# Optimization experiments

Measured on AMD Instinct MI355X. Metric: run time of the kernel, lower is better.

The kernel has to match this reference:

```python
import jax, jax.numpy as jnp
from jax import lax
import numpy as np

DN = ('NCHW', 'OIHW', 'NCHW')

def _conv(x, w, b, s):
    # torch Conv2d(kernel=3, padding=1, stride=s)
    y = lax.conv_general_dilated(x, w, (s, s), ((1, 1), (1, 1)), dimension_numbers=DN)
    return y + b[None, :, None, None]

def _convT(x, w, b, s):
    # torch ConvTranspose2d weight layout [in, out, kh, kw]; kernel=3, padding=1, output_padding=s-1
    wk = jnp.flip(w, (2, 3)).transpose(1, 0, 2, 3)  # -> OIHW
    y = lax.conv_general_dilated(x, wk, (1, 1), ((1, s), (1, s)), lhs_dilation=(s, s), dimension_numbers=DN)
    return y + b[None, :, None, None]

def _inorm(x, eps=1e-5):
    # torch InstanceNorm2d (affine=False)
    m = jnp.mean(x, (2, 3), keepdims=True)
    v = jnp.var(x, (2, 3), keepdims=True)
    return (x - m) * lax.rsqrt(v + eps)

def _prelu(x, a):
    return jnp.where(x >= 0, x, a * x)

def _block(x, w, b, a, s):
    return _prelu(_inorm(_conv(x, w, b, s)), a)

def _sage(x, src, tgt, wl, bl, wr, n):
    # PyG SAGEConv, mean aggregation: lin_l(scatter_mean(x[src] -> tgt)) + lin_r(x)
    deg = jnp.zeros((n,), x.dtype).at[tgt].add(1.0)
    agg = jnp.zeros((x.shape[0], n, x.shape[2]), x.dtype).at[:, tgt].add(x[:, src])
    agg = agg / jnp.maximum(deg, 1.0)[None, :, None]
    return jnp.einsum('bnc,oc->bno', agg, wl) + bl + jnp.einsum('bnc,oc->bno', x, wr)

def setup_inputs() -> dict:
    keys = iter(jax.random.split(jax.random.key(0), 64))
    def rn(shape, s=0.05):
        return jax.random.normal(next(keys), shape, jnp.float32) * s
    inp = {}
    inp['x'] = jax.random.normal(next(keys), (16, 1, 400, 400), jnp.float32)
    inp['edges'] = jax.random.randint(next(keys), (2, 5000), 0, 625, jnp.int32)
    for name, (ci, co) in zip(['d4', 'd3', 'd2', 'd1'], [(1, 32), (32, 64), (64, 128), (128, 256)]):
        inp['w_' + name] = rn((co, ci, 3, 3)); inp['b_' + name] = rn((co,))
        inp['a_' + name] = jnp.full((1,), 0.25, jnp.float32)
    inp['w_bot'] = rn((256, 256, 3, 3)); inp['b_bot'] = rn((256,))
    inp['a_bot'] = jnp.full((1,), 0.25, jnp.float32)
    for i in ['1', '2']:
        inp['wl' + i] = rn((256, 256)); inp['bl' + i] = rn((256,)); inp['wr' + i] = rn((256, 256))
    for name, (ci, co) in zip(['u1', 'u2', 'u3'], [(512, 128), (256, 64), (128, 32)]):
        inp['w_' + name] = rn((ci, co, 3, 3)); inp['b_' + name] = rn((co,))
        inp['a_' + name] = jnp.full((1,), 0.25, jnp.float32)
    inp['w_u4'] = rn((64, 2, 3, 3)); inp['b_u4'] = rn((2,))
    return inp

def reference(x, edges, w_d4, b_d4, a_d4, w_d3, b_d3, a_d3, w_d2, b_d2, a_d2, w_d1, b_d1, a_d1, w_bot, b_bot, a_bot, wl1, bl1, wr1, wl2, bl2, wr2, w_u1, b_u1, a_u1, w_u2, b_u2, a_u2, w_u3, b_u3, a_u3, w_u4, b_u4):
    xs = []
    x = _block(x, w_d4, b_d4, a_d4, 2); xs.append(x)   # [B,32,200,200]
    x = _block(x, w_d3, b_d3, a_d3, 2); xs.append(x)   # [B,64,100,100]
    x = _block(x, w_d2, b_d2, a_d2, 2); xs.append(x)   # [B,128,50,50]
    x = _block(x, w_d1, b_d1, a_d1, 2); xs.append(x)   # [B,256,25,25]
    x = _block(x, w_bot, b_bot, a_bot, 1)              # [B,256,25,25]
    B = x.shape[0]
    x = x.reshape(B, 256, -1).transpose(0, 2, 1)       # [B,625,256]
    src, tgt = edges[0], edges[1]
    x = jax.nn.relu(_sage(x, src, tgt, wl1, bl1, wr1, 625))
    x = jax.nn.relu(_sage(x, src, tgt, wl2, bl2, wr2, 625))
    x = x.transpose(0, 2, 1).reshape(B, 256, 25, 25)
    x = jnp.concatenate([xs[3], x], 1)                 # 512 ch
    x = _prelu(_inorm(_convT(x, w_u1, b_u1, 2)), a_u1) # [B,128,50,50]
    x = jnp.concatenate([xs[2], x], 1)
    x = _prelu(_inorm(_convT(x, w_u2, b_u2, 2)), a_u2) # [B,64,100,100]
    x = jnp.concatenate([xs[1], x], 1)
    x = _prelu(_inorm(_convT(x, w_u3, b_u3, 2)), a_u3) # [B,32,200,200]
    x = jnp.concatenate([xs[0], x], 1)
    return _convT(x, w_u4, b_u4, 2)                    # [B,2,400,400], conv_only top
```

## Files before the change

### kernel.cpp

```cpp
#include <hip/hip_runtime.h>
#include <hip/hip_bf16.h>

typedef __hip_bfloat16 bf16;

typedef __bf16 bf16x8 __attribute__((ext_vector_type(8)));
typedef float  f32x16 __attribute__((ext_vector_type(16)));

static __device__ __forceinline__ float bf(const bf16 v){ return __bfloat162float(v); }
static __device__ __forceinline__ float bfu(unsigned short u){
  unsigned fw = ((unsigned)u) << 16; float v; __builtin_memcpy(&v, &fw, 4); return v;
}

static __device__ __forceinline__ float ldm(const void* p, long i, int f){
  return f ? ((const float*)p)[i] : __bfloat162float(((const bf16*)p)[i]);
}
static __device__ __forceinline__ void stm(void* p, long i, int f, float v){
  if(f) ((float*)p)[i] = v; else ((bf16*)p)[i] = __float2bfloat16(v);
}
static __device__ __forceinline__ unsigned short bfbits(float v){
  __hip_bfloat16 h = __float2bfloat16(v);
  return *(unsigned short*)&h;
}

__global__ void k_detect(const void* __restrict__ w, int* __restrict__ mode){
  if(blockIdx.x == 0 && threadIdx.x == 0){
    const unsigned int* u = (const unsigned int*)w;
    int saneLo = 0;
    for(int i = 0; i < 64; i++){
      unsigned short lo = (unsigned short)(u[i] & 0xFFFFu);
      unsigned int fw = ((unsigned int)lo) << 16;
      float v; __builtin_memcpy(&v, &fw, 4);
      float a = fabsf(v);
      if(a > 1e-7f && a < 100.f) saneLo++;
    }
    *mode = (saneLo >= 48) ? 0 : 1;
  }
}

__global__ void k_wtrans6(const void* __restrict__ w, bf16* __restrict__ wF,
                          const int* __restrict__ dmode){
  int idx = blockIdx.x * 256 + threadIdx.x;
  if(idx >= 65536) return;
  int dm = *dmode;
  int e = idx & 7;
  int L = (idx >> 3) & 63;
  int r = idx >> 9;
  int nc = r & 7;
  int kc = r >> 3;
  int o = nc*32 + (L & 31);
  int c = kc*16 + (L >> 5)*8 + e;
  wF[idx] = __float2bfloat16(ldm(w, (long)o*256 + c, dm));
}

__global__ void k_wtrans4(const void* __restrict__ w, bf16* __restrict__ wF,
                          const int* __restrict__ dmode, int Cin, int Cout){
  int idx = blockIdx.x * 256 + threadIdx.x;
  if(idx >= Cin * Cout * 9) return;
  int dm = *dmode;
  int e = idx & 7;
  int L = (idx >> 3) & 63;
  int r = idx >> 9;
  int NC = Cout >> 5;
  int nc = r % NC; r /= NC;
  int t  = r % 9;
  int kc = r / 9;
  int ci = kc*16 + (L>>5)*8 + e;
  int co = nc*32 + (L&31);
  wF[idx] = __float2bfloat16(ldm(w, ((long)ci*Cout + co)*9 + t, dm));
}

__global__ void k_wtrans5(const void* __restrict__ w, bf16* __restrict__ wF,
                          const int* __restrict__ dmode, int Cin, int Cout){
  int idx = blockIdx.x * 256 + threadIdx.x;
  if(idx >= Cin * Cout * 9) return;
  int dm = *dmode;
  int e = idx & 7;
  int L = (idx >> 3) & 63;
  int r = idx >> 9;
  int NC = Cout >> 5;
  int nc = r % NC; r /= NC;
  int t  = r % 9;
  int kc = r / 9;
  int ci = kc*16 + (L>>5)*8 + e;
  int co = nc*32 + (L&31);
  wF[idx] = __float2bfloat16(ldm(w, ((long)co*Cin + ci)*9 + t, dm));
}

__global__ __launch_bounds__(256, 4)
void k_conv_d4(const void* __restrict__ in, long in_off,
               const void* __restrict__ w, const void* __restrict__ bias,
               bf16* __restrict__ out, const int* __restrict__ dmode)
{
  __shared__ float sW[288];
  __shared__ float sB[32];
  int tid = threadIdx.x;
  int dm = *dmode;
  for(int e = tid; e < 288; e += 256) sW[e] = ldm(w, e, dm);
  if(tid < 32)  sB[tid] = ldm(bias, tid, dm);
  __syncthreads();
  int r = tid / 50, jt = tid % 50;
  if(r >= 5) return;
  int ho = blockIdx.x * 5 + r;
  int b  = blockIdx.z;
  int j0 = jt * 4;

  float x[3][9];
  long ibase = in_off + (long)b * 160000;
  #pragma unroll
  for(int rr = 0; rr < 3; rr++){
    int ir = 2*ho - 1 + rr;
    if(ir < 0 || ir >= 400){
      #pragma unroll
      for(int c = 0; c < 9; c++) x[rr][c] = 0.f;
      continue;
    }
    long rb = ibase + (long)ir * 400;
    int c0 = 2*j0 - 1;
    #pragma unroll
    for(int c = 0; c < 9; c++){
      int ic = c0 + c;
      x[rr][c] = (ic >= 0 && ic < 400) ? ldm(in, rb + ic, dm) : 0.f;
    }
  }

  long obase = ((long)b * 32) * 40000 + (long)ho * 200 + j0;
  for(int co = 0; co < 32; co++){
    const float* wv = &sW[co*9];
    float bv = sB[co];
    float a[4];
    #pragma unroll
    for(int p = 0; p < 4; p++){
      float s = bv;
      #pragma unroll
      for(int kh = 0; kh < 3; kh++)
        #pragma unroll
        for(int kw = 0; kw < 3; kw++)
          s += x[kh][2*p + kw] * wv[kh*3 + kw];
      a[p] = s;
    }
    ushort4 pk;
    pk.x = bfbits(a[0]); pk.y = bfbits(a[1]); pk.z = bfbits(a[2]); pk.w = bfbits(a[3]);
    *(ushort4*)&out[obase + (long)co * 40000] = pk;
  }
}

template<int CW, int NWC, int NWM, int S, int OCC, int VECW>
__global__ __launch_bounds__(256, OCC)
void k_convSM(const void* __restrict__ in, long in_off, int fin_sel,
              const bf16* __restrict__ wF, const void* __restrict__ bias,
              void* __restrict__ out, int fout,
              const int* __restrict__ dmode,
              int Cin, int Hin, int Win, int Cout, int Hout, int Wout, int nym)
{
  constexpr int CP = 40;
  constexpr int HALF = CW/2;
  __shared__ unsigned short sX[3*CW*CP];
  int tid  = threadIdx.x;
  int lane = tid & 63;
  int wv   = tid >> 6;
  int nc   = wv % NWC;
  int mt   = wv / NWC;
  int ho   = blockIdx.x;
  int colg = blockIdx.y % nym;
  int cog  = blockIdx.y / nym;
  int b    = blockIdx.z;
  int dm   = *dmode;
  int fin  = (fin_sel == 2) ? dm : fin_sel;
  int NCtot = Cout >> 5;
  int chunk = cog*NWC + nc;
  int jl   = mt*32 + (lane & 31);
  int hi   = lane >> 5;
  int C0   = S*(colg*NWM*32);
  int ir0  = S*ho - 1;

  f32x16 acc;
  #pragma unroll
  for(int q = 0; q < 16; q++) acc[q] = 0.f;

  int p0, p1, p2;
  if(S == 2){ p0 = jl; p1 = HALF + jl; p2 = jl + 1; }
  else      { p0 = jl; p1 = jl + 1;    p2 = jl + 2; }

  for(int ci0 = 0; ci0 < Cin; ci0 += 32){
    if(VECW == 1){
      for(int e = tid; e < 12*CW; e += 256){
        int c  = e % CW;
        int s  = e / CW;
        int kg = s & 3, r = s >> 2;
        int ir = ir0 + r;
        int ic = C0 - 1 + c;
        unsigned pk0, pk1, pk2, pk3;
        if(ir >= 0 && ir < Hin && ic >= 0 && ic < Win){
          long step = (long)Hin*Win;
          long base = in_off + ((long)b*Cin + ci0 + kg*8)*step + (long)ir*Win + ic;
          unsigned short t8[8];
          #pragma unroll
          for(int u = 0; u < 8; u++) t8[u] = bfbits(ldm(in, base + u*step, fin));
          pk0 = t8[0] | ((unsigned)t8[1]<<16);
          pk1 = t8[2] | ((unsigned)t8[3]<<16);
          pk2 = t8[4] | ((unsigned)t8[5]<<16);
          pk3 = t8[6] | ((unsigned)t8[7]<<16);
        } else { pk0=0; pk1=0; pk2=0; pk3=0; }
        int pos = (S == 2) ? ((c&1) ? HALF + (c>>1) : (c>>1)) : c;
        uint4 q; q.x=pk0; q.y=pk1; q.z=pk2; q.w=pk3;
        *(uint4*)&sX[(r*CW + pos)*CP + kg*8] = q;
      }
    } else {
      const unsigned short* bp = (const unsigned short*)in;
      long step = (long)Hin*Win;
      int L0 = (C0 >= 1) ? ((C0-1) & ~(VECW-1)) : -VECW;
      int ng = (C0 + CW - 2 - L0)/VECW + 1;
      int total = 3 * 8 * ng;
      for(int e = tid; e < total; e += 256){
        int c4 = e & 7;
        int s  = e >> 3;
        int g  = s % ng;
        int r  = s / ng;
        int ir = ir0 + r;
        int L  = L0 + g*VECW;
        int cib = ci0 + c4*4;
        unsigned short t[4][VECW];
        if(ir >= 0 && ir < Hin && L >= 0 && L + VECW <= Win){
          const unsigned short* rp = bp + in_off + ((long)b*Cin + cib)*step + (long)ir*Win + L;
          #pragma unroll
          for(int u = 0; u < 4; u++){
            if(VECW == 4){
              ushort4 v = *(const ushort4*)(rp + u*step);
              t[u][0]=v.x; t[u][1]=v.y; t[u][2]=v.z; t[u][3]=v.w;
            } else {
              ushort2 v = *(const ushort2*)(rp + u*step);
              t[u][0]=v.x; t[u][1]=v.y;
            }
          }
        } else {
          #pragma unroll
          for(int j = 0; j < VECW; j++){
            int ic = L + j;
            bool ok = (ir >= 0 && ir < Hin && ic >= 0 && ic < Win);
            #pragma unroll
            for(int u = 0; u < 4; u++)
              t[u][j] = ok ? bp[in_off + ((long)b*Cin + cib+u)*step + (long)ir*Win + ic]
                           : (unsigned short)0;
          }
        }
        #pragma unroll
        for(int j = 0; j < VECW; j++){
          int c = L - C0 + 1 + j;
          if(c < 0 || c >= CW) continue;
          int pos = (S == 2) ? ((c&1) ? HALF + (c>>1) : (c>>1)) : c;
          uint2 q;
          q.x = t[0][j] | ((unsigned)t[1][j]<<16);
          q.y = t[2][j] | ((unsigned)t[3][j]<<16);
          *(uint2*)&sX[(r*CW + pos)*CP + c4*4] = q;
        }
      }
    }
    __syncthreads();

    #pragma unroll
    for(int kg2 = 0; kg2 < 2; kg2++){
      int kbase = 8*hi + kg2*16;
      bf16x8 x[9];
      #pragma unroll
      for(int r = 0; r < 3; r++){
        x[r*3+0] = *(const bf16x8*)&sX[(r*CW + p0)*CP + kbase];
        x[r*3+1] = *(const bf16x8*)&sX[(r*CW + p1)*CP + kbase];
        x[r*3+2] = *(const bf16x8*)&sX[(r*CW + p2)*CP + kbase];
      }
      int kc = (ci0 >> 4) + kg2;
      const bf16x8* wb = ((const bf16x8*)wF) + ((long)(kc*9)*NCtot + chunk)*64 + lane;
      const long ws = (long)NCtot*64;
      #pragma unroll
      for(int t = 0; t < 9; t++){
        bf16x8 w = wb[(long)t*ws];
        acc = __builtin_amdgcn_mfma_f32_32x32x16_bf16(w, x[t], acc, 0,0,0);
      }
    }
    __syncthreads();
  }

  int j = colg*NWM*32 + jl;
  if(j < Wout){
    #pragma unroll
    for(int r16 = 0; r16 < 16; r16++){
      int co = chunk*32 + (r16&3) + 8*(r16>>2) + 4*hi;
      float bv = ldm(bias, co, dm);
      stm(out, ((long)b*Cout + co)*Hout*Wout + (long)ho*Wout + j, fout, acc[r16] + bv);
    }
  }
}

__global__ void k_inorm_prelu(void* __restrict__ x, int f, int HW,
                              const void* __restrict__ a, const int* __restrict__ dmode)
{
  int dm = *dmode;
  long base = (long)blockIdx.x * HW;
  float s = 0.f, s2 = 0.f;
  int vec = (f == 0) && ((HW & 3) == 0);
  if(vec){
    const ushort4* vp = (const ushort4*)((const bf16*)x + base);
    int n = HW >> 2;
    for(int i = threadIdx.x; i < n; i += 256){
      ushort4 v = vp[i];
      float a0 = bfu(v.x), a1 = bfu(v.y), a2 = bfu(v.z), a3 = bfu(v.w);
      s  += (a0 + a1) + (a2 + a3);
      s2 += (a0*a0 + a1*a1) + (a2*a2 + a3*a3);
    }
  } else {
    for(int i = threadIdx.x; i < HW; i += 256){ float v = ldm(x, base + i, f); s += v; s2 += v*v; }
  }
  __shared__ float sh[256], sh2[256];
  sh[threadIdx.x] = s; sh2[threadIdx.x] = s2; __syncthreads();
  for(int off = 128; off > 0; off >>= 1){
    if(threadIdx.x < off){ sh[threadIdx.x] += sh[threadIdx.x+off]; sh2[threadIdx.x] += sh2[threadIdx.x+off]; }
    __syncthreads();
  }
  float mean = sh[0] / HW;
  float var  = sh2[0] / HW - mean * mean;
  float inv  = rsqrtf(fmaxf(var, 0.f) + 1e-5f);
  float alpha = ldm(a, 0, dm);
  if(vec){
    ushort4* vp = (ushort4*)((bf16*)x + base);
    int n = HW >> 2;
    for(int i = threadIdx.x; i < n; i += 256){
      ushort4 v = vp[i];
      float t[4] = { bfu(v.x), bfu(v.y), bfu(v.z), bfu(v.w) };
      #pragma unroll
      for(int k = 0; k < 4; k++){
        float u = (t[k] - mean) * inv;
        t[k] = u >= 0.f ? u : alpha * u;
      }
      ushort4 o;
      o.x = bfbits(t[0]); o.y = bfbits(t[1]); o.z = bfbits(t[2]); o.w = bfbits(t[3]);
      vp[i] = o;
    }
  } else {
    for(int i = threadIdx.x; i < HW; i += 256){
      float v = (ldm(x, base + i, f) - mean) * inv;
      stm(x, base + i, f, v >= 0.f ? v : alpha * v);
    }
  }
}

__global__ void k_transpose(const float* __restrict__ in, float* __restrict__ out, int B, int C, int N){
  long idx = (long)blockIdx.x * 256 + threadIdx.x;
  long total = (long)B * C * N; if(idx >= total) return;
  int c = (int)(idx % C); long t = idx / C; int n = (int)(t % N); int b = (int)(t / N);
  out[idx] = in[((long)b * C + c) * N + n];
}

__global__ void k_deg(const int* __restrict__ tgt, float* __restrict__ deg, int E){
  int e = blockIdx.x * 256 + threadIdx.x;
  if(e < E) atomicAdd(&deg[tgt[e]], 1.0f);
}

__global__ void k_scatter(const float* __restrict__ xT, const int* __restrict__ src,
                          const int* __restrict__ tgt, float* __restrict__ agg,
                          int E, int C, int N, int B)
{
  int t = blockIdx.x * 256 + threadIdx.x;
  if(t >= E * C) return;
  int c = t % C; int e = t / C;
  int s = src[e], d = tgt[e];
  for(int b = 0; b < B; b++){
    atomicAdd(&agg[((long)b * N + d) * C + c], xT[((long)b * N + s) * C + c]);
  }
}

__global__ __launch_bounds__(256, 4)
void k_sageM(const float* __restrict__ xT, const float* __restrict__ agg,
             const float* __restrict__ deg,
             const bf16* __restrict__ wlF, const bf16* __restrict__ wrF,
             const void* __restrict__ bl,
             float* __restrict__ out, const int* __restrict__ dmode,
             int NROW, int trans)
{
  constexpr int CP = 264;
  __shared__ unsigned short sS[2*32*CP];
  int tid  = threadIdx.x;
  int lane = tid & 63;
  int wv   = tid >> 6;
  int ln   = lane & 31;
  int hi   = lane >> 5;
  int n0   = blockIdx.x * 32;
  int og0  = blockIdx.y * 128;
  int ncg  = blockIdx.y*4 + wv;
  int dm   = *dmode;

  for(int e = tid; e < 4096; e += 256){
    int c4 = e & 63;
    int r  = (e >> 6) & 31;
    int ar = e >> 11;
    int row = n0 + r;
    unsigned pk0 = 0, pk1 = 0;
    if(row < NROW){
      const float* sp = ar ? agg : xT;
      float4 v = *(const float4*)&sp[(long)row*256 + c4*4];
      if(ar){
        int n = row % 625;
        float dinv = 1.0f / fmaxf(deg[n], 1.0f);
        v.x *= dinv; v.y *= dinv; v.z *= dinv; v.w *= dinv;
      }
      pk0 = bfbits(v.x) | ((unsigned)bfbits(v.y) << 16);
      pk1 = bfbits(v.z) | ((unsigned)bfbits(v.w) << 16);
    }
    uint2 q; q.x = pk0; q.y = pk1;
    *(uint2*)&sS[(ar*32 + r)*CP + c4*4] = q;
  }
  __syncthreads();

  f32x16 acc;
  #pragma unroll
  for(int q = 0; q < 16; q++) acc[q] = 0.f;

  int xb = ln*CP + 8*hi;
  #pragma unroll
  for(int kc = 0; kc < 16; kc++){
    bf16x8 bx = *(const bf16x8*)&sS[xb + kc*16];
    bf16x8 ba = *(const bf16x8*)&sS[32*CP + xb + kc*16];
    bf16x8 wl = ((const bf16x8*)wlF)[(long)(kc*8 + ncg)*64 + lane];
    bf16x8 wr = ((const bf16x8*)wrF)[(long)(kc*8 + ncg)*64 + lane];
    acc = __builtin_amdgcn_mfma_f32_32x32x16_bf16(wl, ba, acc, 0,0,0);
    acc = __builtin_amdgcn_mfma_f32_32x32x16_bf16(wr, bx, acc, 0,0,0);
  }

  if(trans){
    int row = n0 + ln;
    if(row < NROW){
      int b = row / 625, n = row - b*625;
      #pragma unroll
      for(int r16 = 0; r16 < 16; r16++){
        int o = ncg*32 + (r16&3) + 8*(r16>>2) + 4*hi;
        float v = acc[r16] + ldm(bl, o, dm);
        out[((long)b*256 + o)*625 + n] = fmaxf(v, 0.f);
      }
    }
  } else {
    float* sO = (float*)sS;
    __syncthreads();
    #pragma unroll
    for(int r16 = 0; r16 < 16; r16++){
      int ol = wv*32 + (r16&3) + 8*(r16>>2) + 4*hi;
      float v = acc[r16] + ldm(bl, og0 + ol, dm);
      sO[ln*130 + ol] = fmaxf(v, 0.f);
    }
    __syncthreads();
    for(int e = tid; e < 4096; e += 256){
      int r = e >> 7, oc = e & 127;
      int row = n0 + r;
      if(row < NROW) out[(long)row*256 + og0 + oc] = sO[r*130 + oc];
    }
  }
}

template<int CW, int NWC, int NWM, int CC, int CIP, int VECW>
__global__ __launch_bounds__(512, 4)
void k_convTG(const void* __restrict__ inA, int fA,
              const void* __restrict__ inB, int fB,
              const bf16* __restrict__ wF, const void* __restrict__ bias,
              bf16* __restrict__ out, const int* __restrict__ dmode,
              int Hin, int Win, int Cout)
{
  __shared__ unsigned short sX[4*CW*CIP];
  int tid  = threadIdx.x;
  int lane = tid & 63;
  int wv   = tid >> 6;
  int low  = wv & 3;
  int h    = wv >> 2;
  int nc   = low % NWC;
  int mt   = low / NWC;
  int j0   = mt * 32;
  int i    = blockIdx.x;
  int b    = blockIdx.z;
  int dm   = *dmode;
  int ln   = lane & 31;
  int hi   = lane >> 5;
  int NCtot = Cout >> 5;

  f32x16 acc0, acc1, acc2, acc3;
  #pragma unroll
  for(int q = 0; q < 16; q++){ acc0[q]=0.f; acc1[q]=0.f; acc2[q]=0.f; acc3[q]=0.f; }

  if(VECW == 1){
    for(int e = tid; e < 4*CW*(CC/8); e += 512){
      int col = e % CW;
      int s   = e / CW;
      int kg  = s % (CC/8); s /= (CC/8);
      int row = s & 1;
      int hf  = s >> 1;
      int ii  = i + row;
      unsigned pk0=0, pk1=0, pk2=0, pk3=0;
      if(ii < Hin && col < Win){
        const void* sp = hf ? inB : inA;
        int ff = hf ? fB : fA;
        long step = (long)Hin*Win;
        long base = ((long)b*CC + kg*8)*step + (long)ii*Win + col;
        unsigned short t8[8];
        #pragma unroll
        for(int u = 0; u < 8; u++) t8[u] = bfbits(ldm(sp, base + u*step, ff));
        pk0 = t8[0] | ((unsigned)t8[1]<<16);
        pk1 = t8[2] | ((unsigned)t8[3]<<16);
        pk2 = t8[4] | ((unsigned)t8[5]<<16);
        pk3 = t8[6] | ((unsigned)t8[7]<<16);
      }
      uint4 q; q.x=pk0; q.y=pk1; q.z=pk2; q.w=pk3;
      *(uint4*)&sX[((hf*2 + row)*CW + col)*CIP + kg*8] = q;
    }
  } else {
    long step = (long)Hin*Win;
    constexpr int NG = (CW + VECW - 1)/VECW;
    constexpr int NC4 = CC/4;
    int total = 4 * NC4 * NG;
    for(int e = tid; e < total; e += 512){
      int c4 = e % NC4;
      int s  = e / NC4;
      int g  = s % NG; s /= NG;
      int row = s & 1;
      int hf  = s >> 1;
      int ii  = i + row;
      int col0 = g*VECW;
      const unsigned short* bp = (const unsigned short*)(hf ? inB : inA);
      unsigned short t[4][VECW];
      if(ii < Hin && col0 + VECW <= Win){
        const unsigned short* rp = bp + ((long)b*CC + c4*4)*step + (long)ii*Win + col0;
        #pragma unroll
        for(int u = 0; u < 4; u++){
          if(VECW == 4){
            ushort4 v = *(const ushort4*)(rp + u*step);
            t[u][0]=v.x; t[u][1]=v.y; t[u][2]=v.z; t[u][3]=v.w;
          } else {
            ushort2 v = *(const ushort2*)(rp + u*step);
            t[u][0]=v.x; t[u][1]=v.y;
          }
        }
      } else {
        #pragma unroll
        for(int j = 0; j < VECW; j++){
          int ic = col0 + j;
          bool ok = (ii < Hin && ic < Win);
          #pragma unroll
          for(int u = 0; u < 4; u++)
            t[u][j] = ok ? bp[((long)b*CC + c4*4+u)*step + (long)ii*Win + ic]
                         : (unsigned short)0;
        }
      }
      #pragma unroll
      for(int j = 0; j < VECW; j++){
        int c = col0 + j;
        if(c >= CW) continue;
        uint2 q;
        q.x = t[0][j] | ((unsigned)t[1][j]<<16);
        q.y = t[2][j] | ((unsigned)t[3][j]<<16);
        *(uint2*)&sX[((hf*2 + row)*CW + c)*CIP + c4*4] = q;
      }
    }
  }
  __syncthreads();

  for(int kc = 0; kc < CC/16; kc++){
    int kb = kc*16 + 8*hi;
    bf16x8 x00 = *(const bf16x8*)&sX[((h*2+0)*CW + j0 + ln)*CIP + kb];
    bf16x8 x01 = *(const bf16x8*)&sX[((h*2+0)*CW + j0 + ln + 1)*CIP + kb];
    bf16x8 x10 = *(const bf16x8*)&sX[((h*2+1)*CW + j0 + ln)*CIP + kb];
    bf16x8 x11 = *(const bf16x8*)&sX[((h*2+1)*CW + j0 + ln + 1)*CIP + kb];
    int kcg = h*(CC/16) + kc;
    const bf16x8* wb = ((const bf16x8*)wF) + ((long)(kcg*9)*NCtot + nc)*64 + lane;
    const int ws = NCtot*64;
    bf16x8 w0=wb[0],    w1=wb[ws],   w2=wb[2*ws], w3=wb[3*ws], w4=wb[4*ws],
           w5=wb[5*ws], w6=wb[6*ws], w7=wb[7*ws], w8=wb[8*ws];
    acc0 = __builtin_amdgcn_mfma_f32_32x32x16_bf16(w4, x00, acc0, 0,0,0);
    acc1 = __builtin_amdgcn_mfma_f32_32x32x16_bf16(w5, x00, acc1, 0,0,0);
    acc1 = __builtin_amdgcn_mfma_f32_32x32x16_bf16(w3, x01, acc1, 0,0,0);
    acc2 = __builtin_amdgcn_mfma_f32_32x32x16_bf16(w7, x00, acc2, 0,0,0);
    acc2 = __builtin_amdgcn_mfma_f32_32x32x16_bf16(w1, x10, acc2, 0,0,0);
    acc3 = __builtin_amdgcn_mfma_f32_32x32x16_bf16(w8, x00, acc3, 0,0,0);
    acc3 = __builtin_amdgcn_mfma_f32_32x32x16_bf16(w6, x01, acc3, 0,0,0);
    acc3 = __builtin_amdgcn_mfma_f32_32x32x16_bf16(w2, x10, acc3, 0,0,0);
    acc3 = __builtin_amdgcn_mfma_f32_32x32x16_bf16(w0, x11, acc3, 0,0,0);
  }

  float* sR = (float*)sX;
  __syncthreads();
  if(h == 1){
    #pragma unroll
    for(int q = 0; q < 16; q++){
      sR[(0*16+q)*256 + low*64 + lane] = acc0[q];
      sR[(1*16+q)*256 + low*64 + lane] = acc1[q];
      sR[(2*16+q)*256 + low*64 + lane] = acc2[q];
      sR[(3*16+q)*256 + low*64 + lane] = acc3[q];
    }
  }
  __syncthreads();
  if(h == 0){
    #pragma unroll
    for(int q = 0; q < 16; q++){
      acc0[q] += sR[(0*16+q)*256 + low*64 + lane];
      acc1[q] += sR[(1*16+q)*256 + low*64 + lane];
      acc2[q] += sR[(2*16+q)*256 + low*64 + lane];
      acc3[q] += sR[(3*16+q)*256 + low*64 + lane];
    }
    int j = j0 + ln;
    if(j < Win){
      int Wout = 2*Win;
      #pragma unroll
      for(int r = 0; r < 16; r++){
        int co = nc*32 + (r&3) + 8*(r>>2) + 4*hi;
        float bv = ldm(bias, co, dm);
        long base0 = (((long)b*Cout + co)*2*Hin + 2*i)*(long)Wout + 2*j;
        unsigned p0 = bfbits(acc0[r]+bv) | ((unsigned)bfbits(acc1[r]+bv) << 16);
        unsigned p1 = bfbits(acc2[r]+bv) | ((unsigned)bfbits(acc3[r]+bv) << 16);
        *(unsigned*)&out[base0]        = p0;
        *(unsigned*)&out[base0 + Wout] = p1;
      }
    }
  }
}

__global__ __launch_bounds__(256, 2)
void k_convT8(const bf16* __restrict__ inA, const bf16* __restrict__ inB,
              const void* __restrict__ w, const void* __restrict__ bias,
              void* __restrict__ out, long out_off, int fout_sel,
              const int* __restrict__ dmode, int Hin, int Win)
{
  __shared__ float sW[64*2*9];
  __shared__ float sB[2];
  int tid = threadIdx.x;
  int dm = *dmode;
  for(int e = tid; e < 64*2*9; e += 256) sW[e] = ldm(w, e, dm);
  if(tid < 2) sB[tid] = ldm(bias, tid, dm);
  __syncthreads();
  int r  = tid / 50;
  int jt = tid % 50;
  if(r >= 5) return;
  int i  = blockIdx.x * 5 + r;
  int b  = blockIdx.z;
  int j0 = jt * 4;
  int fout = (fout_sel == 2) ? dm : fout_sel;

  float acc[2][4][4];
  #pragma unroll
  for(int co = 0; co < 2; co++)
    #pragma unroll
    for(int p = 0; p < 4; p++){
      acc[co][p][0]=0.f; acc[co][p][1]=0.f; acc[co][p][2]=0.f; acc[co][p][3]=0.f;
    }

  bool e4   = (j0 + 4 < Win);
  bool row1 = (i + 1 < Hin);

  for(int ci = 0; ci < 64; ci++){
    const bf16* src = (ci < 32) ? inA : inB;
    int cc = ci & 31;
    const bf16* rp = src + ((long)b*32 + cc)*(long)Hin*Win + (long)i*Win + j0;
    float x0[5], x1[5];
    ushort4 v0 = *(const ushort4*)rp;
    x0[0]=bfu(v0.x); x0[1]=bfu(v0.y); x0[2]=bfu(v0.z); x0[3]=bfu(v0.w);
    x0[4] = e4 ? bf(rp[4]) : 0.f;
    if(row1){
      ushort4 v1 = *(const ushort4*)(rp + Win);
      x1[0]=bfu(v1.x); x1[1]=bfu(v1.y); x1[2]=bfu(v1.z); x1[3]=bfu(v1.w);
      x1[4] = e4 ? bf(rp[Win + 4]) : 0.f;
    } else {
      x1[0]=0.f; x1[1]=0.f; x1[2]=0.f; x1[3]=0.f; x1[4]=0.f;
    }
    const float* wp = &sW[ci*18];
    float wv[18];
    #pragma unroll
    for(int k = 0; k < 18; k++) wv[k] = wp[k];
    #pragma unroll
    for(int p = 0; p < 4; p++){
      float a00 = x0[p], a01 = x0[p+1], a10 = x1[p], a11 = x1[p+1];
      #pragma unroll
      for(int co = 0; co < 2; co++){
        const float* wc = &wv[co*9];
        acc[co][p][0] += a00*wc[4];
        acc[co][p][1] += a00*wc[5] + a01*wc[3];
        acc[co][p][2] += a00*wc[7] + a10*wc[1];
        acc[co][p][3] += a00*wc[8] + a01*wc[6] + a10*wc[2] + a11*wc[0];
      }
    }
  }
  int Wout = 2*Win;
  #pragma unroll
  for(int co = 0; co < 2; co++){
    float bv = sB[co];
    long base = out_off + (((long)b*2 + co)*2*Hin + 2*i)*(long)Wout + 2*j0;
    #pragma unroll
    for(int p = 0; p < 4; p++){
      stm(out, base + 2*p,            fout, acc[co][p][0] + bv);
      stm(out, base + 2*p + 1,        fout, acc[co][p][1] + bv);
      stm(out, base + 2*p + Wout,     fout, acc[co][p][2] + bv);
      stm(out, base + 2*p + Wout + 1, fout, acc[co][p][3] + bv);
    }
  }
}

static inline int cdiv(long a, long b){ return (int)((a + b - 1) / b); }

extern "C" void kernel_launch(void* const* d_in, const int* in_sizes, int n_in,
                              void* d_out, int out_size, void* d_ws, size_t ws_size,
                              hipStream_t stream) {
  const void* x_in  = d_in[0];
  const int*  edges = (const int*)d_in[1];
  const int* src = edges;
  const int* tgt = edges + 5000;
  const void *w_d4=d_in[2],  *b_d4=d_in[3],  *a_d4=d_in[4];
  const void *w_d3=d_in[5],  *b_d3=d_in[6],  *a_d3=d_in[7];
  const void *w_d2=d_in[8],  *b_d2=d_in[9],  *a_d2=d_in[10];
  const void *w_d1=d_in[11], *b_d1=d_in[12], *a_d1=d_in[13];
  const void *w_bot=d_in[14],*b_bot=d_in[15],*a_bot=d_in[16];
  const void *wl1=d_in[17], *bl1=d_in[18], *wr1=d_in[19];
  const void *wl2=d_in[20], *bl2=d_in[21], *wr2=d_in[22];
  const void *w_u1=d_in[23], *b_u1=d_in[24], *a_u1=d_in[25];
  const void *w_u2=d_in[26], *b_u2=d_in[27], *a_u2=d_in[28];
  const void *w_u3=d_in[29], *b_u3=d_in[30], *a_u3=d_in[31];
  const void *w_u4=d_in[32], *b_u4=d_in[33];

  const int NNODE = 625, E = 5000, CG = 256;

  const long TAIL = 4096 + 4*262144L + (589824L + 147456L + 36864L) * 2;
  const long ENCW = 976896L * 2;
  int Bc = 16;
  while(Bc > 1 && (7680000L * Bc + TAIL) > (long)ws_size) Bc >>= 1;
  int enc_in_pool = (Bc >= 8);
  if(!enc_in_pool){
    Bc = 16;
    while(Bc > 1 && (7680000L * Bc + TAIL + ENCW) > (long)ws_size) Bc >>= 1;
  }

  char* wsb = (char*)d_ws;
  long o_xs1  = 2560000L * Bc;
  long o_BIGA = 3840000L * Bc;
  long o_BIGB = 6400000L * Bc;
  long o_deg  = 7680000L * Bc;
  bf16*  xs0 = (bf16*)wsb;
  bf16*  xs1 = (bf16*)(wsb + o_xs1);
  bf16*  xs2 = (bf16*)(wsb + o_BIGA);
  bf16*  xs3 = (bf16*)(wsb + o_BIGA +  640000L*Bc);
  float* bot = (float*)(wsb + o_BIGA +  960000L*Bc);
  float* xT  = (float*)(wsb + o_BIGA + 1600000L*Bc);
  bf16*  u1  = (bf16*)(wsb + o_BIGA + 1600000L*Bc);
  bf16*  u3  = (bf16*)(wsb + o_BIGA);
  float* agg = (float*)(wsb + o_BIGB);
  float* g1  = (float*)(wsb + o_BIGB +  640000L*Bc);
  bf16*  u2  = (bf16*)(wsb + o_BIGB);
  float* deg = (float*)(wsb + o_deg);
  int*  mode = (int*)(wsb + o_deg + 3072);
  bf16*  wlF1 = (bf16*)(wsb + o_deg + 4096);
  bf16*  wrF1 = wlF1 + 65536;
  bf16*  wlF2 = wrF1 + 65536;
  bf16*  wrF2 = wlF2 + 65536;
  bf16*  wTu1 = (bf16*)(wsb + o_deg + 4096 + 4*262144L);
  bf16*  wTu2 = wTu1 + 589824;
  bf16*  wTu3 = wTu2 + 147456;
  bf16*  wTd3 = enc_in_pool ? (bf16*)(wsb + o_BIGA + 2240000L*Bc) : (wTu3 + 36864);
  bf16*  wTd2 = wTd3 + 18432;
  bf16*  wTd1 = wTd2 + 73728;
  bf16*  wTdB = wTd1 + 294912;
  float* g2  = bot;

  hipLaunchKernelGGL(k_detect, dim3(1), dim3(1), 0, stream, w_d4, mode);

  hipMemsetAsync(deg, 0, NNODE*sizeof(float), stream);
  hipLaunchKernelGGL(k_deg, dim3(cdiv(E,256)), dim3(256), 0, stream, tgt, deg, E);
  hipLaunchKernelGGL(k_wtrans6, dim3(256), dim3(256), 0, stream, wl1, wlF1, mode);
  hipLaunchKernelGGL(k_wtrans6, dim3(256), dim3(256), 0, stream, wr1, wrF1, mode);
  hipLaunchKernelGGL(k_wtrans6, dim3(256), dim3(256), 0, stream, wl2, wlF2, mode);
  hipLaunchKernelGGL(k_wtrans6, dim3(256), dim3(256), 0, stream, wr2, wrF2, mode);
  hipLaunchKernelGGL(k_wtrans4, dim3(cdiv(589824,256)), dim3(256), 0, stream, w_u1, wTu1, mode, 512, 128);
  hipLaunchKernelGGL(k_wtrans4, dim3(cdiv(147456,256)), dim3(256), 0, stream, w_u2, wTu2, mode, 256, 64);
  hipLaunchKernelGGL(k_wtrans4, dim3(cdiv(36864,256)),  dim3(256), 0, stream, w_u3, wTu3, mode, 128, 32);

  for(int bo = 0; bo < 16; bo += Bc){
    long x_off   = (long)bo * 160000;
    long out_off = (long)bo * 320000;

    hipLaunchKernelGGL(k_wtrans5, dim3(cdiv(18432,256)),  dim3(256), 0, stream, w_d3, wTd3, mode, 32, 64);
    hipLaunchKernelGGL(k_wtrans5, dim3(cdiv(73728,256)),  dim3(256), 0, stream, w_d2, wTd2, mode, 64, 128);
    hipLaunchKernelGGL(k_wtrans5, dim3(cdiv(294912,256)), dim3(256), 0, stream, w_d1, wTd1, mode, 128, 256);
    hipLaunchKernelGGL(k_wtrans5, dim3(cdiv(589824,256)), dim3(256), 0, stream, w_bot, wTdB, mode, 256, 256);

    hipLaunchKernelGGL(k_conv_d4, dim3(40, 1, Bc), dim3(256), 0, stream,
                       x_in, x_off, w_d4, b_d4, xs0, mode);
    hipLaunchKernelGGL(k_inorm_prelu, dim3(Bc*32), dim3(256), 0, stream, xs0, 0, 40000, a_d4, mode);
    hipLaunchKernelGGL((k_convSM<130,2,2,2,4,4>), dim3(100, 2, Bc), dim3(256), 0, stream,
                       xs0, 0L, 0, wTd3, b_d3, xs1, 0, mode, 32, 200, 200, 64, 100, 100, 2);
    hipLaunchKernelGGL(k_inorm_prelu, dim3(Bc*64), dim3(256), 0, stream, xs1, 0, 10000, a_d3, mode);
    hipLaunchKernelGGL((k_convSM<66,4,1,2,4,4>), dim3(50, 2, Bc), dim3(256), 0, stream,
                       xs1, 0L, 0, wTd2, b_d2, xs2, 0, mode, 64, 100, 100, 128, 50, 50, 2);
    hipLaunchKernelGGL(k_inorm_prelu, dim3(Bc*128), dim3(256), 0, stream, xs2, 0, 2500, a_d2, mode);
    hipLaunchKernelGGL((k_convSM<66,4,1,2,4,2>), dim3(25, 2, Bc), dim3(256), 0, stream,
                       xs2, 0L, 0, wTd1, b_d1, xs3, 0, mode, 128, 50, 50, 256, 25, 25, 1);
    hipLaunchKernelGGL(k_inorm_prelu, dim3(Bc*256), dim3(256), 0, stream, xs3, 0, 625, a_d1, mode);
    hipLaunchKernelGGL((k_convSM<34,4,1,1,4,1>), dim3(25, 2, Bc), dim3(256), 0, stream,
                       xs3, 0L, 0, wTdB, b_bot, bot, 1, mode, 256, 25, 25, 256, 25, 25, 1);
    hipLaunchKernelGGL(k_inorm_prelu, dim3(Bc*256), dim3(256), 0, stream, bot, 1, 625, a_bot, mode);

    { long n = (long)Bc*CG*NNODE;
      hipLaunchKernelGGL(k_transpose, dim3(cdiv(n,256)), dim3(256), 0, stream, bot, xT, Bc, CG, NNODE); }
    hipMemsetAsync(agg, 0, 640000L*Bc, stream);
    hipLaunchKernelGGL(k_scatter, dim3(cdiv((long)E*CG,256)), dim3(256), 0, stream, xT, src, tgt, agg, E, CG, NNODE, Bc);
    hipLaunchKernelGGL(k_sageM, dim3(cdiv((long)Bc*NNODE,32), 2), dim3(256), 0, stream,
                       xT, agg, deg, wlF1, wrF1, bl1, g1, mode, Bc*NNODE, 0);
    hipMemsetAsync(agg, 0, 640000L*Bc, stream);
    hipLaunchKernelGGL(k_scatter, dim3(cdiv((long)E*CG,256)), dim3(256), 0, stream, g1, src, tgt, agg, E, CG, NNODE, Bc);
    hipLaunchKernelGGL(k_sageM, dim3(cdiv((long)Bc*NNODE,32), 2), dim3(256), 0, stream,
                       g1, agg, deg, wlF2, wrF2, bl2, g2, mode, Bc*NNODE, 1);

    hipLaunchKernelGGL((k_convTG<34,4,1,256,264,1>), dim3(25, 1, Bc), dim3(512), 0, stream,
                       xs3, 0, g2, 1, wTu1, b_u1, u1, mode, 25, 25, 128);
    hipLaunchKernelGGL(k_inorm_prelu, dim3(Bc*128), dim3(256), 0, stream, u1, 0, 2500, a_u1, mode);
    hipLaunchKernelGGL((k_convTG<66,2,2,128,136,2>), dim3(50, 1, Bc), dim3(512), 0, stream,
                       xs2, 0, u1, 0, wTu2, b_u2, u2, mode, 50, 50, 64);
    hipLaunchKernelGGL(k_inorm_prelu, dim3(Bc*64), dim3(256), 0, stream, u2, 0, 10000, a_u2, mode);
    hipLaunchKernelGGL((k_convTG<130,1,4,64,72,4>), dim3(100, 1, Bc), dim3(512), 0, stream,
                       xs1, 0, u2, 0, wTu3, b_u3, u3, mode, 100, 100, 32);
    hipLaunchKernelGGL(k_inorm_prelu, dim3(Bc*32), dim3(256), 0, stream, u3, 0, 40000, a_u3, mode);
    hipLaunchKernelGGL(k_convT8, dim3(40, 1, Bc), dim3(256), 0, stream,
                       xs0, u3, w_u4, b_u4, d_out, out_off, 2, mode, 200, 200);
  }
}
```

Measured before the change: 900.4 us.

## Replace atomic scatter-mean with CSR gather fused into SAGE GEMM kernel

Builds a CSR (offsets plus source indices sorted by target) once per call via count, serial scan and place kernels. The SAGE kernel then gathers and averages neighbour features directly while staging its tile, which removes the per-layer agg memset, the float atomic scatter over all batches and the deg buffer. It also raises the launch-bounds occupancy hint on the final transposed conv. The risks are a single-thread scan and load imbalance, because the neighbour count per row varies inside the staging loop.

```diff
diff --git a/kernel.cpp b/kernel.cpp
--- a/kernel.cpp
+++ b/kernel.cpp
@@ -84,6 +84,28 @@
   int ci = kc*16 + (L>>5)*8 + e;
   int co = nc*32 + (L&31);
   wF[idx] = __float2bfloat16(ldm(w, ((long)co*Cin + ci)*9 + t, dm));
+}
+
+__global__ void k_count(const int* __restrict__ tgt, int* __restrict__ icur, int E){
+  int e = blockIdx.x * 256 + threadIdx.x;
+  if(e < E) atomicAdd(&icur[tgt[e]], 1);
+}
+__global__ void k_scan(int* __restrict__ icur, int* __restrict__ off, int N){
+  if(blockIdx.x == 0 && threadIdx.x == 0){
+    int acc = 0;
+    for(int i = 0; i < N; i++){ off[i] = acc; acc += icur[i]; icur[i] = 0; }
+    off[N] = acc;
+  }
+}
+__global__ void k_place(const int* __restrict__ src, const int* __restrict__ tgt,
+                        const int* __restrict__ off, int* __restrict__ icur,
+                        int* __restrict__ eidx, int E){
+  int e = blockIdx.x * 256 + threadIdx.x;
+  if(e < E){
+    int d = tgt[e];
+    int p = atomicAdd(&icur[d], 1);
+    eidx[off[d] + p] = src[e];
+  }
 }
 
 __global__ __launch_bounds__(256, 4)
@@ -349,27 +371,9 @@
   out[idx] = in[((long)b * C + c) * N + n];
 }
 
-__global__ void k_deg(const int* __restrict__ tgt, float* __restrict__ deg, int E){
-  int e = blockIdx.x * 256 + threadIdx.x;
-  if(e < E) atomicAdd(&deg[tgt[e]], 1.0f);
-}
-
-__global__ void k_scatter(const float* __restrict__ xT, const int* __restrict__ src,
-                          const int* __restrict__ tgt, float* __restrict__ agg,
-                          int E, int C, int N, int B)
-{
-  int t = blockIdx.x * 256 + threadIdx.x;
-  if(t >= E * C) return;
-  int c = t % C; int e = t / C;
-  int s = src[e], d = tgt[e];
-  for(int b = 0; b < B; b++){
-    atomicAdd(&agg[((long)b * N + d) * C + c], xT[((long)b * N + s) * C + c]);
-  }
-}
-
 __global__ __launch_bounds__(256, 4)
-void k_sageM(const float* __restrict__ xT, const float* __restrict__ agg,
-             const float* __restrict__ deg,
+void k_sageG(const float* __restrict__ xT,
+             const int* __restrict__ off, const int* __restrict__ eidx,
              const bf16* __restrict__ wlF, const bf16* __restrict__ wrF,
              const void* __restrict__ bl,
              float* __restrict__ out, const int* __restrict__ dmode,
@@ -394,11 +398,21 @@
     int row = n0 + r;
     unsigned pk0 = 0, pk1 = 0;
     if(row < NROW){
-      const float* sp = ar ? agg : xT;
-      float4 v = *(const float4*)&sp[(long)row*256 + c4*4];
-      if(ar){
-        int n = row % 625;
-        float dinv = 1.0f / fmaxf(deg[n], 1.0f);
+      float4 v;
+      if(ar == 0){
+        v = *(const float4*)&xT[(long)row*256 + c4*4];
+      } else {
+        int b = row / 625;
+        int n = row - b*625;
+        int s0 = off[n], s1 = off[n+1];
+        v.x = 0.f; v.y = 0.f; v.z = 0.f; v.w = 0.f;
+        long bb = (long)b*625*256 + c4*4;
+        for(int k = s0; k < s1; k++){
+          int s = eidx[k];
+          float4 u = *(const float4*)&xT[bb + (long)s*256];
+          v.x += u.x; v.y += u.y; v.z += u.z; v.w += u.w;
+        }
+        float dinv = 1.0f / fmaxf((float)(s1 - s0), 1.0f);
         v.x *= dinv; v.y *= dinv; v.z *= dinv; v.w *= dinv;
       }
       pk0 = bfbits(v.x) | ((unsigned)bfbits(v.y) << 16);
@@ -616,7 +630,7 @@
   }
 }
 
-__global__ __launch_bounds__(256, 2)
+__global__ __launch_bounds__(256, 4)
 void k_convT8(const bf16* __restrict__ inA, const bf16* __restrict__ inB,
               const void* __restrict__ w, const void* __restrict__ bias,
               void* __restrict__ out, long out_off, int fout_sel,
@@ -718,7 +732,7 @@
 
   const int NNODE = 625, E = 5000, CG = 256;
 
-  const long TAIL = 4096 + 4*262144L + (589824L + 147456L + 36864L) * 2;
+  const long TAIL = 4096 + 4*262144L + (589824L + 147456L + 36864L) * 2 + 32768;
   const long ENCW = 976896L * 2;
   int Bc = 16;
   while(Bc > 1 && (7680000L * Bc + TAIL) > (long)ws_size) Bc >>= 1;
@@ -741,10 +755,8 @@
   float* xT  = (float*)(wsb + o_BIGA + 1600000L*Bc);
   bf16*  u1  = (bf16*)(wsb + o_BIGA + 1600000L*Bc);
   bf16*  u3  = (bf16*)(wsb + o_BIGA);
-  float* agg = (float*)(wsb + o_BIGB);
   float* g1  = (float*)(wsb + o_BIGB +  640000L*Bc);
   bf16*  u2  = (bf16*)(wsb + o_BIGB);
-  float* deg = (float*)(wsb + o_deg);
   int*  mode = (int*)(wsb + o_deg + 3072);
   bf16*  wlF1 = (bf16*)(wsb + o_deg + 4096);
   bf16*  wrF1 = wlF1 + 65536;
@@ -753,7 +765,10 @@
   bf16*  wTu1 = (bf16*)(wsb + o_deg + 4096 + 4*262144L);
   bf16*  wTu2 = wTu1 + 589824;
   bf16*  wTu3 = wTu2 + 147456;
-  bf16*  wTd3 = enc_in_pool ? (bf16*)(wsb + o_BIGA + 2240000L*Bc) : (wTu3 + 36864);
+  int*   ioff = (int*)(wTu3 + 36864);
+  int*   icur = ioff + 626;
+  int*   eidx = icur + 625;
+  bf16*  wTd3 = enc_in_pool ? (bf16*)(wsb + o_BIGA + 2240000L*Bc) : (bf16*)(eidx + 5000);
   bf16*  wTd2 = wTd3 + 18432;
   bf16*  wTd1 = wTd2 + 73728;
   bf16*  wTdB = wTd1 + 294912;
@@ -761,8 +776,11 @@
 
   hipLaunchKernelGGL(k_detect, dim3(1), dim3(1), 0, stream, w_d4, mode);
 
-  hipMemsetAsync(deg, 0, NNODE*sizeof(float), stream);
-  hipLaunchKernelGGL(k_deg, dim3(cdiv(E,256)), dim3(256), 0, stream, tgt, deg, E);
+  hipMemsetAsync(icur, 0, NNODE*sizeof(int), stream);
+  hipLaunchKernelGGL(k_count, dim3(cdiv(E,256)), dim3(256), 0, stream, tgt, icur, E);
+  hipLaunchKernelGGL(k_scan,  dim3(1), dim3(64), 0, stream, icur, ioff, NNODE);
+  hipLaunchKernelGGL(k_place, dim3(cdiv(E,256)), dim3(256), 0, stream, src, tgt, ioff, icur, eidx, E);
+
   hipLaunchKernelGGL(k_wtrans6, dim3(256), dim3(256), 0, stream, wl1, wlF1, mode);
   hipLaunchKernelGGL(k_wtrans6, dim3(256), dim3(256), 0, stream, wr1, wrF1, mode);
   hipLaunchKernelGGL(k_wtrans6, dim3(256), dim3(256), 0, stream, wl2, wlF2, mode);
@@ -798,14 +816,10 @@
 
     { long n = (long)Bc*CG*NNODE;
       hipLaunchKernelGGL(k_transpose, dim3(cdiv(n,256)), dim3(256), 0, stream, bot, xT, Bc, CG, NNODE); }
-    hipMemsetAsync(agg, 0, 640000L*Bc, stream);
-    hipLaunchKernelGGL(k_scatter, dim3(cdiv((long)E*CG,256)), dim3(256), 0, stream, xT, src, tgt, agg, E, CG, NNODE, Bc);
-    hipLaunchKernelGGL(k_sageM, dim3(cdiv((long)Bc*NNODE,32), 2), dim3(256), 0, stream,
-                       xT, agg, deg, wlF1, wrF1, bl1, g1, mode, Bc*NNODE, 0);
-    hipMemsetAsync(agg, 0, 640000L*Bc, stream);
-    hipLaunchKernelGGL(k_scatter, dim3(cdiv((long)E*CG,256)), dim3(256), 0, stream, g1, src, tgt, agg, E, CG, NNODE, Bc);
-    hipLaunchKernelGGL(k_sageM, dim3(cdiv((long)Bc*NNODE,32), 2), dim3(256), 0, stream,
-                       g1, agg, deg, wlF2, wrF2, bl2, g2, mode, Bc*NNODE, 1);
+    hipLaunchKernelGGL(k_sageG, dim3(cdiv((long)Bc*NNODE,32), 2), dim3(256), 0, stream,
+                       xT, ioff, eidx, wlF1, wrF1, bl1, g1, mode, Bc*NNODE, 0);
+    hipLaunchKernelGGL(k_sageG, dim3(cdiv((long)Bc*NNODE,32), 2), dim3(256), 0, stream,
+                       g1, ioff, eidx, wlF2, wrF2, bl2, g2, mode, Bc*NNODE, 1);
 
     hipLaunchKernelGGL((k_convTG<34,4,1,256,264,1>), dim3(25, 1, Bc), dim3(512), 0, stream,
                        xs3, 0, g2, 1, wTu1, b_u1, u1, mode, 25, 25, 128);
```

Result: no change. 904.0 us, median of 2 (+0.4%).
